# Performance work log

Hardware: AMD Instinct MI355X
Metric: run time of the kernel (lower is better)

## Reference

```python
import jax, jax.numpy as jnp
import numpy as np

E = 262144      # number of edges (triples)
D = 256         # embed_dim
DOUT = 256      # embed_out_dim
NQ = 65536      # num_query (output nodes)
NK = 65536      # num_key
ALPHA = 0.2     # leaky relu slope
EPS = 1e-12


def setup_inputs() -> dict:
    key = jax.random.key(0)
    ks = jax.random.split(key, 7)
    return {
        "key_list": jax.random.randint(ks[0], (E,), 0, NK),
        "key_embed": jax.random.normal(ks[1], (E, D), jnp.float32),
        "query_list": jax.random.randint(ks[2], (E,), 0, NQ),
        "query_embed": jax.random.normal(ks[3], (E, D), jnp.float32),
        # learned parameters (xavier-ish scale)
        "a": jax.random.normal(ks[4], (DOUT, 2 * D), jnp.float32) * 0.05,
        "a_2": jax.random.normal(ks[5], (1, DOUT), jnp.float32) * 0.05,
        "trans": jax.random.normal(ks[6], (DOUT, D), jnp.float32) * 0.05,
    }


def reference(key_list, key_embed, query_list, query_embed, a, a_2, trans):
    # edge_associated_set = trans @ key_embed.T, kept as (E, DOUT)
    edge_assoc = key_embed @ trans.T                              # (E, DOUT)
    # edge_m = a @ cat(key, query).T, kept as (E, DOUT)
    edge_h = jnp.concatenate([key_embed, query_embed], axis=1)    # (E, 2D)
    edge_m = edge_h @ a.T                                         # (E, DOUT)
    powers = -jax.nn.leaky_relu(edge_m @ a_2[0], negative_slope=ALPHA)  # (E,)
    edge_e = jnp.exp(powers)                                      # (E,) unnormalized attn
    # sparse COO sum over key dim == segment-sum by query index
    e_rowsum = jax.ops.segment_sum(edge_e, query_list, num_segments=NQ)[:, None]  # (NQ,1)
    e_rowsum = jnp.where(e_rowsum == 0.0, EPS, e_rowsum)
    # dropout p=0.0 (eval) -> identity
    edge_w = edge_e[:, None] * edge_assoc                         # (E, DOUT)
    h_prime = jax.ops.segment_sum(edge_w, query_list, num_segments=NQ)  # (NQ, DOUT)
    h_prime = h_prime / e_rowsum
    return jax.nn.elu(h_prime)  # concat=True branch
```

## Files before the change

kernel.cpp:

```cpp
#include <hip/hip_runtime.h>
#include <hip/hip_bf16.h>
#include <math.h>

namespace {
constexpr int kD = 256;
constexpr int kDOUT = 256;
constexpr int kNQ = 65536;
constexpr int kE = 262144;
constexpr float kAlpha = 0.2f;
constexpr float kEps = 1e-12f;
constexpr int kCap = 16;
constexpr int kOvfMax = 4096;
}

typedef short bf16x8 __attribute__((ext_vector_type(8)));
typedef float f32x4 __attribute__((ext_vector_type(4)));
typedef unsigned short u16x8 __attribute__((ext_vector_type(8)));

__global__ __launch_bounds__(256) void prep_kernel(
    const float* __restrict__ a,
    const float* __restrict__ a2,
    const float* __restrict__ trans,
    int4* __restrict__ count4,
    int* __restrict__ ovf_n,
    float* __restrict__ c,
    ushort* __restrict__ tb) {
  const int b = blockIdx.x;
  const int tid = threadIdx.x;
  if (b < 64) {
    count4[b * 256 + tid] = int4{0, 0, 0, 0};
    if (b == 0 && tid == 0) *ovf_n = 0;
  } else if (b < 66) {
    const int j = (b - 64) * 256 + tid;
    float s = 0.f;
#pragma unroll 8
    for (int k = 0; k < kDOUT; ++k) s = fmaf(a[k * (2 * kD) + j], a2[k], s);
    c[j] = s;
  } else {
    const int i = (b - 66) * 256 + tid;
    const float4 v = reinterpret_cast<const float4*>(trans)[i];
    union { ushort4 u; __hip_bfloat16 h[4]; } p;
    p.h[0] = __float2bfloat16(v.x);
    p.h[1] = __float2bfloat16(v.y);
    p.h[2] = __float2bfloat16(v.z);
    p.h[3] = __float2bfloat16(v.w);
    reinterpret_cast<ushort4*>(tb)[i] = p.u;
  }
}

__global__ __launch_bounds__(256) void qdot_bin_kernel(
    const float* __restrict__ query_embed,
    const int* __restrict__ qlist,
    const float* __restrict__ c,
    int* __restrict__ count,
    int2* __restrict__ bins,
    int* __restrict__ ovf_n,
    int* __restrict__ ovf_q,
    int* __restrict__ ovf_e,
    float* __restrict__ ovf_qd) {
  const int wid = threadIdx.x >> 6;
  const int lane = threadIdx.x & 63;
  const int g = lane >> 4;
  const int l4 = lane & 15;
  const int edge = blockIdx.x * 16 + wid * 4 + g;

  int q = 0;
  if (l4 == 0) q = qlist[edge];

  const float4* qr = reinterpret_cast<const float4*>(query_embed) + (size_t)edge * 64 + l4 * 4;
  const float4 r0 = qr[0], r1 = qr[1], r2 = qr[2], r3 = qr[3];
  const float4 c0 = reinterpret_cast<const float4*>(c)[64 + l4 * 4 + 0];
  const float4 c1 = reinterpret_cast<const float4*>(c)[64 + l4 * 4 + 1];
  const float4 c2 = reinterpret_cast<const float4*>(c)[64 + l4 * 4 + 2];
  const float4 c3 = reinterpret_cast<const float4*>(c)[64 + l4 * 4 + 3];

  float s = r0.x * c0.x + r0.y * c0.y + r0.z * c0.z + r0.w * c0.w
          + r1.x * c1.x + r1.y * c1.y + r1.z * c1.z + r1.w * c1.w
          + r2.x * c2.x + r2.y * c2.y + r2.z * c2.z + r2.w * c2.w
          + r3.x * c3.x + r3.y * c3.y + r3.z * c3.z + r3.w * c3.w;
#pragma unroll
  for (int off = 1; off < 16; off <<= 1) s += __shfl_xor(s, off, 64);

  if (l4 == 0) {
    const int slot = atomicAdd(&count[q], 1);
    if (slot < kCap) {
      bins[q * kCap + slot] = make_int2(edge, __float_as_int(s));
    } else {
      const int o = atomicAdd(ovf_n, 1);
      if (o < kOvfMax) { ovf_q[o] = q; ovf_e[o] = edge; ovf_qd[o] = s; }
    }
  }
}

__global__ __launch_bounds__(256) void gather_gemm_kernel(
    const float* __restrict__ key_embed,
    const float* __restrict__ c,
    const int2* __restrict__ bins,
    const int* __restrict__ count,
    const int* __restrict__ ovf_n,
    const int* __restrict__ ovf_q,
    const int* __restrict__ ovf_e,
    const float* __restrict__ ovf_qd,
    const ushort* __restrict__ B,
    float* __restrict__ out) {
  __shared__ ushort A_lds[32][264];
  const int wid = threadIdx.x >> 6;
  const int lane = threadIdx.x & 63;
  const int g = lane >> 4;
  const int l4 = lane & 15;
  const int group = wid * 4 + g;

  const float4 ck0 = reinterpret_cast<const float4*>(c)[l4 * 4 + 0];
  const float4 ck1 = reinterpret_cast<const float4*>(c)[l4 * 4 + 1];
  const float4 ck2 = reinterpret_cast<const float4*>(c)[l4 * 4 + 2];
  const float4 ck3 = reinterpret_cast<const float4*>(c)[l4 * 4 + 3];

  for (int half = 0; half < 2; ++half) {
    const int qloc = half * 16 + group;
    const int q = blockIdx.x * 32 + qloc;
    const int cnt = count[q];
    const int cm = min(cnt, kCap);
    const int2 mybin = (l4 < cm) ? bins[q * kCap + l4] : make_int2(0, 0);

    float acc[16] = {};
    float rs = 0.f;

    for (int s = 0; s < cm; s += 4) {
      const int kc = min(4, cm - s);
      float4 r[4][4];
      float qd[4];
#pragma unroll
      for (int t = 0; t < 4; ++t) {
        if (t < kc) {
          const int eg = __shfl(mybin.x, (g << 4) + s + t, 64);
          qd[t] = __int_as_float(__shfl(mybin.y, (g << 4) + s + t, 64));
          const float4* row = reinterpret_cast<const float4*>(key_embed) + (size_t)eg * 64 + l4 * 4;
#pragma unroll
          for (int u = 0; u < 4; ++u) r[t][u] = row[u];
        }
      }
#pragma unroll
      for (int t = 0; t < 4; ++t) {
        if (t < kc) {
          float kd = r[t][0].x * ck0.x + r[t][0].y * ck0.y + r[t][0].z * ck0.z + r[t][0].w * ck0.w
                   + r[t][1].x * ck1.x + r[t][1].y * ck1.y + r[t][1].z * ck1.z + r[t][1].w * ck1.w
                   + r[t][2].x * ck2.x + r[t][2].y * ck2.y + r[t][2].z * ck2.z + r[t][2].w * ck2.w
                   + r[t][3].x * ck3.x + r[t][3].y * ck3.y + r[t][3].z * ck3.z + r[t][3].w * ck3.w;
#pragma unroll
          for (int off = 1; off < 16; off <<= 1) kd += __shfl_xor(kd, off, 64);
          const float sv = kd + qd[t];
          const float p = (sv > 0.f) ? sv : kAlpha * sv;
          const float ev = __expf(-p);
#pragma unroll
          for (int u = 0; u < 4; ++u) {
            acc[u * 4 + 0] = fmaf(ev, r[t][u].x, acc[u * 4 + 0]);
            acc[u * 4 + 1] = fmaf(ev, r[t][u].y, acc[u * 4 + 1]);
            acc[u * 4 + 2] = fmaf(ev, r[t][u].z, acc[u * 4 + 2]);
            acc[u * 4 + 3] = fmaf(ev, r[t][u].w, acc[u * 4 + 3]);
          }
          rs += ev;
        }
      }
    }

    if (cnt > kCap) {
      const int n = min(*ovf_n, kOvfMax);
      for (int i = 0; i < n; ++i) {
        if (ovf_q[i] == q) {
          const float4* row = reinterpret_cast<const float4*>(key_embed) +
                              (size_t)ovf_e[i] * 64 + l4 * 4;
          float4 r4[4];
#pragma unroll
          for (int u = 0; u < 4; ++u) r4[u] = row[u];
          float kd = r4[0].x * ck0.x + r4[0].y * ck0.y + r4[0].z * ck0.z + r4[0].w * ck0.w
                   + r4[1].x * ck1.x + r4[1].y * ck1.y + r4[1].z * ck1.z + r4[1].w * ck1.w
                   + r4[2].x * ck2.x + r4[2].y * ck2.y + r4[2].z * ck2.z + r4[2].w * ck2.w
                   + r4[3].x * ck3.x + r4[3].y * ck3.y + r4[3].z * ck3.z + r4[3].w * ck3.w;
#pragma unroll
          for (int off = 1; off < 16; off <<= 1) kd += __shfl_xor(kd, off, 64);
          const float sv = kd + ovf_qd[i];
          const float p = (sv > 0.f) ? sv : kAlpha * sv;
          const float ev = __expf(-p);
#pragma unroll
          for (int u = 0; u < 4; ++u) {
            acc[u * 4 + 0] = fmaf(ev, r4[u].x, acc[u * 4 + 0]);
            acc[u * 4 + 1] = fmaf(ev, r4[u].y, acc[u * 4 + 1]);
            acc[u * 4 + 2] = fmaf(ev, r4[u].z, acc[u * 4 + 2]);
            acc[u * 4 + 3] = fmaf(ev, r4[u].w, acc[u * 4 + 3]);
          }
          rs += ev;
        }
      }
    }

    const float inv = 1.0f / ((rs == 0.f) ? kEps : rs);
    union { u16x8 u; __hip_bfloat16 h[8]; } p0, p1;
#pragma unroll
    for (int j = 0; j < 8; ++j) p0.h[j] = __float2bfloat16(acc[j] * inv);
#pragma unroll
    for (int j = 0; j < 8; ++j) p1.h[j] = __float2bfloat16(acc[8 + j] * inv);
    *reinterpret_cast<u16x8*>(&A_lds[qloc][l4 * 16]) = p0.u;
    *reinterpret_cast<u16x8*>(&A_lds[qloc][l4 * 16 + 8]) = p1.u;
  }

  __syncthreads();

  const int m = lane & 15;
  const int kb = (lane >> 4) * 8;
  f32x4 accA[4] = {};
  f32x4 accB[4] = {};

#pragma unroll
  for (int kt = 0; kt < kD; kt += 32) {
    const bf16x8 af0 = *reinterpret_cast<const bf16x8*>(&A_lds[m][kt + kb]);
    const bf16x8 af1 = *reinterpret_cast<const bf16x8*>(&A_lds[16 + m][kt + kb]);
#pragma unroll
    for (int nt = 0; nt < 4; ++nt) {
      const int ntg = wid * 4 + nt;
      const bf16x8 bf =
          *reinterpret_cast<const bf16x8*>(&B[(size_t)(ntg * 16 + m) * kD + kt + kb]);
      accA[nt] = __builtin_amdgcn_mfma_f32_16x16x32_bf16(af0, bf, accA[nt], 0, 0, 0);
      accB[nt] = __builtin_amdgcn_mfma_f32_16x16x32_bf16(af1, bf, accB[nt], 0, 0, 0);
    }
  }

#pragma unroll
  for (int nt = 0; nt < 4; ++nt) {
    const int ntg = wid * 4 + nt;
#pragma unroll
    for (int r = 0; r < 4; ++r) {
      const int rbase = blockIdx.x * 32 + (lane >> 4) * 4 + r;
      const float xa = accA[nt][r];
      out[(size_t)rbase * kDOUT + ntg * 16 + m] = (xa > 0.f) ? xa : expm1f(xa);
      const float xb = accB[nt][r];
      out[(size_t)(rbase + 16) * kDOUT + ntg * 16 + m] = (xb > 0.f) ? xb : expm1f(xb);
    }
  }
}

extern "C" void kernel_launch(void* const* d_in, const int* in_sizes, int n_in,
                              void* d_out, int out_size, void* d_ws, size_t ws_size,
                              hipStream_t stream) {
  const float* key_embed = (const float*)d_in[1];
  const int* query_list = (const int*)d_in[2];
  const float* query_embed = (const float*)d_in[3];
  const float* a = (const float*)d_in[4];
  const float* a2 = (const float*)d_in[5];
  const float* trans = (const float*)d_in[6];
  float* out = (float*)d_out;

  float* ws = (float*)d_ws;
  float* c = ws;
  int* count = (int*)(c + 512);
  int2* bins = (int2*)(count + kNQ);
  ushort* transb = (ushort*)(bins + (size_t)kNQ * kCap);
  int* ovf_n = (int*)(transb + (size_t)kDOUT * kD);
  int* ovf_q = ovf_n + 4;
  int* ovf_e = ovf_q + kOvfMax;
  float* ovf_qd = (float*)(ovf_e + kOvfMax);

  prep_kernel<<<130, 256, 0, stream>>>(a, a2, trans, (int4*)count, ovf_n, c, transb);
  qdot_bin_kernel<<<kE / 16, 256, 0, stream>>>(query_embed, query_list, c, count,
                                               bins, ovf_n, ovf_q, ovf_e, ovf_qd);
  gather_gemm_kernel<<<kNQ / 32, 256, 0, stream>>>(key_embed, c, bins, count, ovf_n,
                                                   ovf_q, ovf_e, ovf_qd, transb, out);
}
```

Baseline: 199.6 us.

## Assign one wavefront per query in gather phase with fixed unrolled edge loop

The gather phase now maps each wavefront to 8 queries, processed one at a time with all 64 lanes covering a full 256-float row (one float4 per lane), instead of 16-lane groups reading four float4s each. It preloads bin entries for all 8 queries, then runs a fully unrolled 8-slot loop with clamped indices and masked exps so the row loads can be issued back to back, followed by a remainder loop for counts above 8. The intent is more independent memory requests in flight and fully coalesced row reads. In exchange, the dot-product reduction becomes a 64-lane shuffle tree, and queries with fewer than 8 edges still pay for redundant clamped loads and shuffles.

Result: faster. 188.8 us (-5.4%).

```diff
diff --git a/kernel.cpp b/kernel.cpp
--- a/kernel.cpp
+++ b/kernel.cpp
@@ -106,101 +106,92 @@
   __shared__ ushort A_lds[32][264];
   const int wid = threadIdx.x >> 6;
   const int lane = threadIdx.x & 63;
-  const int g = lane >> 4;
-  const int l4 = lane & 15;
-  const int group = wid * 4 + g;
-
-  const float4 ck0 = reinterpret_cast<const float4*>(c)[l4 * 4 + 0];
-  const float4 ck1 = reinterpret_cast<const float4*>(c)[l4 * 4 + 1];
-  const float4 ck2 = reinterpret_cast<const float4*>(c)[l4 * 4 + 2];
-  const float4 ck3 = reinterpret_cast<const float4*>(c)[l4 * 4 + 3];
-
-  for (int half = 0; half < 2; ++half) {
-    const int qloc = half * 16 + group;
-    const int q = blockIdx.x * 32 + qloc;
-    const int cnt = count[q];
-    const int cm = min(cnt, kCap);
-    const int2 mybin = (l4 < cm) ? bins[q * kCap + l4] : make_int2(0, 0);
-
-    float acc[16] = {};
+  const int qbase = blockIdx.x * 32 + wid * 8;
+
+  const float4 ck = reinterpret_cast<const float4*>(c)[lane];
+
+  const int cnt_l = (lane < 8) ? count[qbase + lane] : 0;
+  int2 b[8];
+  int cnts[8];
+#pragma unroll
+  for (int i = 0; i < 8; ++i) {
+    cnts[i] = __shfl(cnt_l, i, 64);
+    const int cmi = min(cnts[i], kCap);
+    b[i] = (lane < cmi) ? bins[(size_t)(qbase + i) * kCap + lane] : make_int2(0, 0);
+  }
+
+#pragma unroll
+  for (int i = 0; i < 8; ++i) {
+    const int cnt_i = cnts[i];
+    const int cmi = min(cnt_i, kCap);
+    const int cl = max(cmi - 1, 0);
+    float4 acc = {0.f, 0.f, 0.f, 0.f};
     float rs = 0.f;
 
-    for (int s = 0; s < cm; s += 4) {
-      const int kc = min(4, cm - s);
-      float4 r[4][4];
-      float qd[4];
-#pragma unroll
-      for (int t = 0; t < 4; ++t) {
-        if (t < kc) {
-          const int eg = __shfl(mybin.x, (g << 4) + s + t, 64);
-          qd[t] = __int_as_float(__shfl(mybin.y, (g << 4) + s + t, 64));
-          const float4* row = reinterpret_cast<const float4*>(key_embed) + (size_t)eg * 64 + l4 * 4;
-#pragma unroll
-          for (int u = 0; u < 4; ++u) r[t][u] = row[u];
-        }
-      }
-#pragma unroll
-      for (int t = 0; t < 4; ++t) {
-        if (t < kc) {
-          float kd = r[t][0].x * ck0.x + r[t][0].y * ck0.y + r[t][0].z * ck0.z + r[t][0].w * ck0.w
-                   + r[t][1].x * ck1.x + r[t][1].y * ck1.y + r[t][1].z * ck1.z + r[t][1].w * ck1.w
-                   + r[t][2].x * ck2.x + r[t][2].y * ck2.y + r[t][2].z * ck2.z + r[t][2].w * ck2.w
-                   + r[t][3].x * ck3.x + r[t][3].y * ck3.y + r[t][3].z * ck3.z + r[t][3].w * ck3.w;
-#pragma unroll
-          for (int off = 1; off < 16; off <<= 1) kd += __shfl_xor(kd, off, 64);
-          const float sv = kd + qd[t];
-          const float p = (sv > 0.f) ? sv : kAlpha * sv;
-          const float ev = __expf(-p);
-#pragma unroll
-          for (int u = 0; u < 4; ++u) {
-            acc[u * 4 + 0] = fmaf(ev, r[t][u].x, acc[u * 4 + 0]);
-            acc[u * 4 + 1] = fmaf(ev, r[t][u].y, acc[u * 4 + 1]);
-            acc[u * 4 + 2] = fmaf(ev, r[t][u].z, acc[u * 4 + 2]);
-            acc[u * 4 + 3] = fmaf(ev, r[t][u].w, acc[u * 4 + 3]);
-          }
+#pragma unroll
+    for (int s = 0; s < 8; ++s) {
+      const int sc = min(s, cl);
+      const int eg = __shfl(b[i].x, sc, 64);
+      const float qd = __int_as_float(__shfl(b[i].y, sc, 64));
+      const float4 k4 = reinterpret_cast<const float4*>(key_embed)[(size_t)eg * 64 + lane];
+      float d = k4.x * ck.x + k4.y * ck.y + k4.z * ck.z + k4.w * ck.w;
+#pragma unroll
+      for (int off = 1; off < 64; off <<= 1) d += __shfl_xor(d, off, 64);
+      const float sv = d + qd;
+      const float pl = (sv > 0.f) ? sv : kAlpha * sv;
+      const float ev = (s < cmi) ? __expf(-pl) : 0.f;
+      acc.x = fmaf(ev, k4.x, acc.x);
+      acc.y = fmaf(ev, k4.y, acc.y);
+      acc.z = fmaf(ev, k4.z, acc.z);
+      acc.w = fmaf(ev, k4.w, acc.w);
+      rs += ev;
+    }
+
+    for (int s = 8; s < cmi; ++s) {
+      const int eg = __shfl(b[i].x, s, 64);
+      const float qd = __int_as_float(__shfl(b[i].y, s, 64));
+      const float4 k4 = reinterpret_cast<const float4*>(key_embed)[(size_t)eg * 64 + lane];
+      float d = k4.x * ck.x + k4.y * ck.y + k4.z * ck.z + k4.w * ck.w;
+#pragma unroll
+      for (int off = 1; off < 64; off <<= 1) d += __shfl_xor(d, off, 64);
+      const float sv = d + qd;
+      const float pl = (sv > 0.f) ? sv : kAlpha * sv;
+      const float ev = __expf(-pl);
+      acc.x = fmaf(ev, k4.x, acc.x);
+      acc.y = fmaf(ev, k4.y, acc.y);
+      acc.z = fmaf(ev, k4.z, acc.z);
+      acc.w = fmaf(ev, k4.w, acc.w);
+      rs += ev;
+    }
+
+    if (cnt_i > kCap) {
+      const int q = qbase + i;
+      const int n = min(*ovf_n, kOvfMax);
+      for (int o = 0; o < n; ++o) {
+        if (ovf_q[o] == q) {
+          const float4 k4 = reinterpret_cast<const float4*>(key_embed)[(size_t)ovf_e[o] * 64 + lane];
+          float d = k4.x * ck.x + k4.y * ck.y + k4.z * ck.z + k4.w * ck.w;
+#pragma unroll
+          for (int off = 1; off < 64; off <<= 1) d += __shfl_xor(d, off, 64);
+          const float sv = d + ovf_qd[o];
+          const float pl = (sv > 0.f) ? sv : kAlpha * sv;
+          const float ev = __expf(-pl);
+          acc.x = fmaf(ev, k4.x, acc.x);
+          acc.y = fmaf(ev, k4.y, acc.y);
+          acc.z = fmaf(ev, k4.z, acc.z);
+          acc.w = fmaf(ev, k4.w, acc.w);
           rs += ev;
         }
       }
     }
 
-    if (cnt > kCap) {
-      const int n = min(*ovf_n, kOvfMax);
-      for (int i = 0; i < n; ++i) {
-        if (ovf_q[i] == q) {
-          const float4* row = reinterpret_cast<const float4*>(key_embed) +
-                              (size_t)ovf_e[i] * 64 + l4 * 4;
-          float4 r4[4];
-#pragma unroll
-          for (int u = 0; u < 4; ++u) r4[u] = row[u];
-          float kd = r4[0].x * ck0.x + r4[0].y * ck0.y + r4[0].z * ck0.z + r4[0].w * ck0.w
-                   + r4[1].x * ck1.x + r4[1].y * ck1.y + r4[1].z * ck1.z + r4[1].w * ck1.w
-                   + r4[2].x * ck2.x + r4[2].y * ck2.y + r4[2].z * ck2.z + r4[2].w * ck2.w
-                   + r4[3].x * ck3.x + r4[3].y * ck3.y + r4[3].z * ck3.z + r4[3].w * ck3.w;
-#pragma unroll
-          for (int off = 1; off < 16; off <<= 1) kd += __shfl_xor(kd, off, 64);
-          const float sv = kd + ovf_qd[i];
-          const float p = (sv > 0.f) ? sv : kAlpha * sv;
-          const float ev = __expf(-p);
-#pragma unroll
-          for (int u = 0; u < 4; ++u) {
-            acc[u * 4 + 0] = fmaf(ev, r4[u].x, acc[u * 4 + 0]);
-            acc[u * 4 + 1] = fmaf(ev, r4[u].y, acc[u * 4 + 1]);
-            acc[u * 4 + 2] = fmaf(ev, r4[u].z, acc[u * 4 + 2]);
-            acc[u * 4 + 3] = fmaf(ev, r4[u].w, acc[u * 4 + 3]);
-          }
-          rs += ev;
-        }
-      }
-    }
-
     const float inv = 1.0f / ((rs == 0.f) ? kEps : rs);
-    union { u16x8 u; __hip_bfloat16 h[8]; } p0, p1;
-#pragma unroll
-    for (int j = 0; j < 8; ++j) p0.h[j] = __float2bfloat16(acc[j] * inv);
-#pragma unroll
-    for (int j = 0; j < 8; ++j) p1.h[j] = __float2bfloat16(acc[8 + j] * inv);
-    *reinterpret_cast<u16x8*>(&A_lds[qloc][l4 * 16]) = p0.u;
-    *reinterpret_cast<u16x8*>(&A_lds[qloc][l4 * 16 + 8]) = p1.u;
+    union { ushort4 u; __hip_bfloat16 h[4]; } pk;
+    pk.h[0] = __float2bfloat16(acc.x * inv);
+    pk.h[1] = __float2bfloat16(acc.y * inv);
+    pk.h[2] = __float2bfloat16(acc.z * inv);
+    pk.h[3] = __float2bfloat16(acc.w * inv);
+    *reinterpret_cast<ushort4*>(&A_lds[wid * 8 + i][lane * 4]) = pk.u;
   }
 
   __syncthreads();
```
